# Kernel optimization log

Measured on AMD Instinct MI355X. Metric: run time of the kernel, lower is better.

The kernel has to match this reference:

```python
import jax, jax.numpy as jnp
import numpy as np

B, G, H1, H2, P, A = 8192, 20000, 512, 256, 128, 64


def setup_inputs() -> dict:
    key = jax.random.key(0)
    ks = jax.random.split(key, 9)
    s = lambda k, shape, fan: jax.random.normal(k, shape, jnp.float32) / np.sqrt(fan)
    return {
        "x": jax.random.normal(ks[0], (B, G), jnp.float32),
        "W1": s(ks[1], (H1, G), G),
        "b1": s(ks[2], (H1,), G),
        "W2": s(ks[3], (H2, H1), H1),
        "b2": s(ks[4], (H2,), H1),
        "W3": s(ks[5], (P, H2, A), H2),
        "b3": s(ks[6], (P, A), H2),
        "W4": s(ks[7], (P, A), A),
        "b4": s(ks[8], (P,), A),
    }


def reference(x, W1, b1, W2, b2, W3, b3, W4, b4):
    # shared trunk: two dense layers with ReLU (torch Linear: y = x @ W.T + b)
    h = jax.nn.relu(x @ W1.T + b1)          # [B, 512]
    h = jax.nn.relu(h @ W2.T + b2)          # [B, 256]
    # per-protein heads, batched over the protein dim P (replaces python loop)
    a = jax.nn.relu(jnp.einsum("bh,pha->bpa", h, W3) + b3)  # [B, P, A]
    out = jnp.einsum("bpa,pa->bp", a, W4) + b4               # [B, P]
    return out
```

## Files before the change

kernel.cpp:

```cpp
#include <hip/hip_runtime.h>
#include <hip/hip_bf16.h>
#include <stdint.h>

typedef unsigned short u16;
typedef __attribute__((ext_vector_type(8))) short short8;
typedef __attribute__((ext_vector_type(8))) u16   u16x8;
typedef __attribute__((ext_vector_type(4))) u16   u16x4;
typedef __attribute__((ext_vector_type(4))) float f32x4;

#define B_DIM  8192
#define G_DIM  20000
#define H1_DIM 512
#define H2_DIM 256
#define P_DIM  128
#define A_DIM  64
#define SPLITK 8
#define NKT_ALL 625

union Frag { short8 s; u16x8 u; };

__device__ __forceinline__ u16 f2b(float f) {
  union { __hip_bfloat16 b; u16 u; } c;
  c.b = __float2bfloat16(f);
  return c.u;
}

__device__ __forceinline__ void gld16(const void* g, void* l) {
  __builtin_amdgcn_global_load_lds(
      (const __attribute__((address_space(1))) void*)g,
      (__attribute__((address_space(3))) void*)l, 16, 0, 0);
}

__global__ void k_convert(const float* __restrict__ src, u16* __restrict__ dst, int n4) {
  int i = blockIdx.x * 256 + threadIdx.x;
  if (i >= n4) return;
  f32x4 v = ((const f32x4*)src)[i];
  u16x4 o;
  o[0] = f2b(v[0]); o[1] = f2b(v[1]);
  o[2] = f2b(v[2]); o[3] = f2b(v[3]);
  ((u16x4*)dst)[i] = o;
}

__global__ void k_convert_w1frag(const float* __restrict__ W1, u16* __restrict__ W1f) {
  int ot = blockIdx.x * 256 + threadIdx.x;
  if (ot >= (H1_DIM / 16) * NKT_ALL * 64) return;
  int rowblk = ot / (NKT_ALL * 64);
  int rem    = ot - rowblk * (NKT_ALL * 64);
  int kt     = rem >> 6;
  int lane   = rem & 63;
  int row = rowblk * 16 + (lane & 15);
  int col = kt * 32 + (lane >> 4) * 8;
  const float* src = W1 + (size_t)row * G_DIM + col;
  f32x4 v0 = *(const f32x4*)src;
  f32x4 v1 = *(const f32x4*)(src + 4);
  u16x8 o;
#pragma unroll
  for (int i = 0; i < 4; ++i) { o[i] = f2b(v0[i]); o[i + 4] = f2b(v1[i]); }
  ((u16x8*)W1f)[ot] = o;
}

__global__ void k_transpose_w3(const float* __restrict__ W3, u16* __restrict__ W3T) {
  int idx = blockIdx.x * 256 + threadIdx.x;
  if (idx >= P_DIM * H2_DIM * A_DIM) return;
  int h = idx & (H2_DIM - 1);
  int a = (idx >> 8) & (A_DIM - 1);
  int p = idx >> 14;
  W3T[idx] = f2b(W3[((size_t)p * H2_DIM + h) * A_DIM + a]);
}

__global__ __launch_bounds__(512, 4)
void k_gemm1(const float* __restrict__ X, const u16* __restrict__ W1f,
             float* __restrict__ partial) {
  const int ks = blockIdx.x & 7;
  const int m0 = (blockIdx.x >> 3) * 64;
  const int kt_begin = (ks == 0) ? 0 : (ks * 78 + 1);
  const int nkt = (ks == 0) ? 79 : 78;

  const int tid  = threadIdx.x;
  const int lane = tid & 63;
  const int w    = tid >> 6;
  const int c15 = lane & 15, j4 = lane >> 4;
  const int w4 = w * 4;

  __shared__ u16 lsA[2][64 * 32];

  const int aRow = tid >> 3;
  const int aG   = tid & 7;
  const int aPhysU16 = aRow * 32 + (((aG >> 1) ^ ((aRow >> 1) & 3)) << 3) + ((aG & 1) << 2);
  const float* aSrc0 = X + (size_t)(m0 + aRow) * G_DIM + aG * 4;

  f32x4 zero = {0.f, 0.f, 0.f, 0.f};
  f32x4 acc[4][4];
#pragma unroll
  for (int m = 0; m < 4; ++m)
#pragma unroll
    for (int n = 0; n < 4; ++n) acc[m][n] = zero;

  auto ktc = [&](int t) { return kt_begin + (t < nkt ? t : nkt - 1); };

  auto loadA = [&](int kt, f32x4& ar) {
    ar = *(const f32x4*)(aSrc0 + (size_t)kt * 32);
  };
  auto writeA = [&](int buf, const f32x4& ar) {
    u16x4 o;
    o[0] = f2b(ar[0]); o[1] = f2b(ar[1]); o[2] = f2b(ar[2]); o[3] = f2b(ar[3]);
    *(u16x4*)&lsA[buf][aPhysU16] = o;
  };

  f32x4 arE, arO;

  loadA(ktc(0), arE);
  loadA(ktc(1), arO);
  writeA(0, arE);
  asm volatile("s_waitcnt vmcnt(1) lgkmcnt(0)" ::: "memory");
  __builtin_amdgcn_s_barrier();
  __builtin_amdgcn_sched_barrier(0);

  auto body = [&](int t, int buf, f32x4& arLoad, const f32x4& arWrite) {
    const int kt = kt_begin + t;
    Frag bfr[4];
#pragma unroll
    for (int n = 0; n < 4; ++n)
      bfr[n].s = *(const short8*)(W1f + ((size_t)((w4 + n) * NKT_ALL + kt) * 64 + lane) * 8);
    loadA(ktc(t + 2), arLoad);

    Frag afr[4];
#pragma unroll
    for (int m = 0; m < 4; ++m) {
      int row = m * 16 + c15;
      int phys = j4 ^ ((row >> 1) & 3);
      afr[m].s = *(const short8*)&lsA[buf][row * 32 + phys * 8];
    }
    writeA(buf ^ 1, arWrite);

#pragma unroll
    for (int m = 0; m < 4; ++m)
#pragma unroll
      for (int n = 0; n < 4; ++n)
        acc[m][n] = __builtin_amdgcn_mfma_f32_16x16x32_bf16(afr[m].s, bfr[n].s, acc[m][n], 0, 0, 0);

    asm volatile("s_waitcnt vmcnt(1) lgkmcnt(0)" ::: "memory");
    __builtin_amdgcn_s_barrier();
    __builtin_amdgcn_sched_barrier(0);
  };

  int t = 0;
  for (; t + 1 < nkt; t += 2) {
    body(t,     0, arE, arO);
    body(t + 1, 1, arO, arE);
  }
  if (t < nkt) body(t, 0, arE, arO);

  float* outp = partial + ((size_t)ks * B_DIM + m0) * H1_DIM;
#pragma unroll
  for (int m = 0; m < 4; ++m)
#pragma unroll
    for (int n = 0; n < 4; ++n)
#pragma unroll
      for (int r = 0; r < 4; ++r) {
        int row = m * 16 + j4 * 4 + r;
        int col = w * 64 + n * 16 + c15;
        outp[(size_t)row * H1_DIM + col] = acc[m][n][r];
      }
}

__global__ void k_reduce1(const float* __restrict__ partial, const float* __restrict__ b1,
                          u16* __restrict__ h1b) {
  const int n4 = B_DIM * H1_DIM / 4;
  int i = blockIdx.x * 256 + threadIdx.x;
  if (i >= n4) return;
  f32x4 s = ((const f32x4*)partial)[i];
#pragma unroll
  for (int k = 1; k < SPLITK; ++k) {
    f32x4 v = ((const f32x4*)partial)[(size_t)k * n4 + i];
    s[0] += v[0]; s[1] += v[1]; s[2] += v[2]; s[3] += v[3];
  }
  f32x4 bb = ((const f32x4*)b1)[i & (H1_DIM / 4 - 1)];
  u16x4 o;
#pragma unroll
  for (int j = 0; j < 4; ++j)
    o[j] = f2b(fmaxf(s[j] + bb[j], 0.f));
  ((u16x4*)h1b)[i] = o;
}

__global__ __launch_bounds__(256, 2)
void k_gemm2(const u16* __restrict__ h1b, const u16* __restrict__ W2b,
             const float* __restrict__ b2, u16* __restrict__ h2b) {
  const int m0 = blockIdx.x * 128;
  const int n0 = blockIdx.y * 64;
  const int tid  = threadIdx.x;
  const int lane = tid & 63;
  const int wid  = tid >> 6;
  const int wr = wid >> 1, wc = wid & 1;
  const int c15 = lane & 15, j4 = lane >> 4;

  __shared__ u16 lsA[2][128 * 32];
  __shared__ u16 lsB[2][64 * 32];

  f32x4 zero = {0.f, 0.f, 0.f, 0.f};
  f32x4 acc[4][2];
#pragma unroll
  for (int m = 0; m < 4; ++m) { acc[m][0] = zero; acc[m][1] = zero; }

  auto stage = [&](int buf, int kt) {
    const int k0 = kt * 32;
#pragma unroll
    for (int c = 0; c < 2; ++c) {
      int lin = c * 256 + tid;
      int row = lin >> 2, slot = lin & 3;
      int gslot = slot ^ ((row >> 1) & 3);
      gld16(h1b + (size_t)(m0 + row) * H1_DIM + k0 + gslot * 8, &lsA[buf][lin * 8]);
    }
    {
      int lin = tid;
      int row = lin >> 2, slot = lin & 3;
      int gslot = slot ^ ((row >> 1) & 3);
      gld16(W2b + (size_t)(n0 + row) * H1_DIM + k0 + gslot * 8, &lsB[buf][lin * 8]);
    }
  };

  stage(0, 0);
  __syncthreads();
  int buf = 0;
  const int nkt = H1_DIM / 32;
  for (int t = 0; t < nkt; ++t) {
    if (t + 1 < nkt) stage(buf ^ 1, t + 1);
    Frag bfr[2];
#pragma unroll
    for (int n = 0; n < 2; ++n) {
      int row = wc * 32 + n * 16 + c15;
      int slot = j4 ^ ((row >> 1) & 3);
      bfr[n].s = *(const short8*)&lsB[buf][row * 32 + slot * 8];
    }
    Frag afr[4];
#pragma unroll
    for (int m = 0; m < 4; ++m) {
      int row = wr * 64 + m * 16 + c15;
      int slot = j4 ^ ((row >> 1) & 3);
      afr[m].s = *(const short8*)&lsA[buf][row * 32 + slot * 8];
    }
#pragma unroll
    for (int m = 0; m < 4; ++m)
#pragma unroll
      for (int n = 0; n < 2; ++n)
        acc[m][n] = __builtin_amdgcn_mfma_f32_16x16x32_bf16(afr[m].s, bfr[n].s, acc[m][n], 0, 0, 0);
    __syncthreads();
    buf ^= 1;
  }

  float b2v[2];
  b2v[0] = b2[n0 + wc * 32 + c15];
  b2v[1] = b2[n0 + wc * 32 + 16 + c15];
#pragma unroll
  for (int m = 0; m < 4; ++m)
#pragma unroll
    for (int n = 0; n < 2; ++n)
#pragma unroll
      for (int r = 0; r < 4; ++r) {
        int row = m0 + wr * 64 + m * 16 + j4 * 4 + r;
        int col = n0 + wc * 32 + n * 16 + c15;
        h2b[(size_t)row * H2_DIM + col] = f2b(fmaxf(acc[m][n][r] + b2v[n], 0.f));
      }
}

__global__ __launch_bounds__(256, 2)
void k_heads(const u16* __restrict__ h2b, const u16* __restrict__ W3T,
             const float* __restrict__ b3, const float* __restrict__ W4,
             const float* __restrict__ b4, float* __restrict__ out) {
  const int m0 = blockIdx.x * 128;
  const int p0 = blockIdx.y * 2;
  const int tid  = threadIdx.x;
  const int lane = tid & 63;
  const int wid  = tid >> 6;
  const int wr = wid >> 1, wc = wid & 1;
  const int c15 = lane & 15, j4 = lane >> 4;

  __shared__ u16 lsA[2][128 * 64];
  __shared__ u16 lsB[2][128 * 64];

  f32x4 zero = {0.f, 0.f, 0.f, 0.f};
  f32x4 acc[4][4];
#pragma unroll
  for (int m = 0; m < 4; ++m)
#pragma unroll
    for (int n = 0; n < 4; ++n) acc[m][n] = zero;

  auto stage = [&](int buf, int kt) {
    const int k0 = kt * 64;
#pragma unroll
    for (int c = 0; c < 4; ++c) {
      int lin = c * 256 + tid;
      int row = lin >> 3, slot = lin & 7;
      int gslot = slot ^ (row & 7);
      gld16(h2b + (size_t)(m0 + row) * H2_DIM + k0 + gslot * 8, &lsA[buf][lin * 8]);
    }
#pragma unroll
    for (int c = 0; c < 4; ++c) {
      int lin = c * 256 + tid;
      int row = lin >> 3, slot = lin & 7;
      int gslot = slot ^ (row & 7);
      gld16(W3T + ((size_t)(p0 * 64 + row)) * H2_DIM + k0 + gslot * 8, &lsB[buf][lin * 8]);
    }
  };

  stage(0, 0);
  __syncthreads();
  int buf = 0;
  const int nkt = H2_DIM / 64;
  for (int t = 0; t < nkt; ++t) {
    if (t + 1 < nkt) stage(buf ^ 1, t + 1);
#pragma unroll
    for (int kk = 0; kk < 2; ++kk) {
      Frag bfr[4];
#pragma unroll
      for (int n = 0; n < 4; ++n) {
        int row = wc * 64 + n * 16 + c15;
        int slot = (kk * 4 + j4) ^ (row & 7);
        bfr[n].s = *(const short8*)&lsB[buf][row * 64 + slot * 8];
      }
      Frag afr[4];
#pragma unroll
      for (int m = 0; m < 4; ++m) {
        int row = wr * 64 + m * 16 + c15;
        int slot = (kk * 4 + j4) ^ (row & 7);
        afr[m].s = *(const short8*)&lsA[buf][row * 64 + slot * 8];
      }
#pragma unroll
      for (int m = 0; m < 4; ++m)
#pragma unroll
        for (int n = 0; n < 4; ++n)
          acc[m][n] = __builtin_amdgcn_mfma_f32_16x16x32_bf16(afr[m].s, bfr[n].s, acc[m][n], 0, 0, 0);
    }
    __syncthreads();
    buf ^= 1;
  }

  const int p = p0 + wc;
  float w4v[4], b3v[4];
#pragma unroll
  for (int n = 0; n < 4; ++n) {
    w4v[n] = W4[p * A_DIM + n * 16 + c15];
    b3v[n] = b3[p * A_DIM + n * 16 + c15];
  }
  const float b4v = b4[p];

  float s[4][4];
#pragma unroll
  for (int m = 0; m < 4; ++m)
#pragma unroll
    for (int r = 0; r < 4; ++r) s[m][r] = 0.f;
#pragma unroll
  for (int m = 0; m < 4; ++m)
#pragma unroll
    for (int n = 0; n < 4; ++n)
#pragma unroll
      for (int r = 0; r < 4; ++r) {
        float v = fmaxf(acc[m][n][r] + b3v[n], 0.f);
        s[m][r] += v * w4v[n];
      }
#pragma unroll
  for (int m = 0; m < 4; ++m)
#pragma unroll
    for (int r = 0; r < 4; ++r) {
      float v = s[m][r];
      v += __shfl_xor(v, 1);
      v += __shfl_xor(v, 2);
      v += __shfl_xor(v, 4);
      v += __shfl_xor(v, 8);
      s[m][r] = v;
    }
  if (c15 == 0) {
#pragma unroll
    for (int m = 0; m < 4; ++m)
#pragma unroll
      for (int r = 0; r < 4; ++r) {
        int row = m0 + wr * 64 + m * 16 + j4 * 4 + r;
        out[(size_t)row * P_DIM + p] = s[m][r] + b4v;
      }
  }
}

extern "C" void kernel_launch(void* const* d_in, const int* in_sizes, int n_in,
                              void* d_out, int out_size, void* d_ws, size_t ws_size,
                              hipStream_t stream) {
  const float* x  = (const float*)d_in[0];
  const float* W1 = (const float*)d_in[1];
  const float* b1 = (const float*)d_in[2];
  const float* W2 = (const float*)d_in[3];
  const float* b2 = (const float*)d_in[4];
  const float* W3 = (const float*)d_in[5];
  const float* b3 = (const float*)d_in[6];
  const float* W4 = (const float*)d_in[7];
  const float* b4 = (const float*)d_in[8];
  float* out = (float*)d_out;

  char* ws = (char*)d_ws;
  u16*   W1f  = (u16*)(ws);
  u16*   W2b  = (u16*)(ws + 20480000);
  u16*   W3T  = (u16*)(ws + 20742144);
  u16*   h1b  = (u16*)(ws + 24936448);
  u16*   h2b  = (u16*)(ws + 33325056);
  float* part = (float*)(ws + 37519360);

  k_convert_w1frag<<<dim3((1280000 + 255) / 256), dim3(256), 0, stream>>>(W1, W1f);
  k_convert<<<dim3(131072 / 4 / 256), dim3(256), 0, stream>>>(W2, W2b, 131072 / 4);
  k_transpose_w3<<<dim3(2097152 / 256), dim3(256), 0, stream>>>(W3, W3T);

  k_gemm1<<<dim3(128 * SPLITK), dim3(512), 0, stream>>>(x, W1f, part);
  k_reduce1<<<dim3(B_DIM * H1_DIM / 4 / 256), dim3(256), 0, stream>>>(part, b1, h1b);
  k_gemm2<<<dim3(64, 4), dim3(256), 0, stream>>>(h1b, W2b, b2, h2b);
  k_heads<<<dim3(64, 64), dim3(256), 0, stream>>>(h2b, W3T, b3, W4, b4, out);
}
```

Before: 374.3 us.

## Double the GEMM1 K-step per barrier and software-pipeline W1 fragment loads

Restructures the split-K GEMM1 main loop so each iteration stages a 64-wide K slab of X in LDS (two 32-wide k-tiles) using a new 8-way XOR swizzle. This halves the number of block barriers. It also double-buffers the B (W1) fragments in registers, so the next tile's weights load while the current MFMAs run. It uses more LDS and VGPRs, and the fixed 39-iteration count with a tail case for nkt==79 must match the split exactly.

```diff
diff --git a/kernel.cpp b/kernel.cpp
--- a/kernel.cpp
+++ b/kernel.cpp
@@ -82,12 +82,12 @@
   const int c15 = lane & 15, j4 = lane >> 4;
   const int w4 = w * 4;
 
-  __shared__ u16 lsA[2][64 * 32];
+  __shared__ u16 lsA[2][64 * 64];
 
   const int aRow = tid >> 3;
   const int aG   = tid & 7;
-  const int aPhysU16 = aRow * 32 + (((aG >> 1) ^ ((aRow >> 1) & 3)) << 3) + ((aG & 1) << 2);
-  const float* aSrc0 = X + (size_t)(m0 + aRow) * G_DIM + aG * 4;
+  const int aPhysU16 = aRow * 64 + ((aG ^ (aRow & 7)) * 8);
+  const float* aSrc0 = X + (size_t)(m0 + aRow) * G_DIM + aG * 8;
 
   f32x4 zero = {0.f, 0.f, 0.f, 0.f};
   f32x4 acc[4][4];
@@ -96,60 +96,84 @@
 #pragma unroll
     for (int n = 0; n < 4; ++n) acc[m][n] = zero;
 
-  auto ktc = [&](int t) { return kt_begin + (t < nkt ? t : nkt - 1); };
-
-  auto loadA = [&](int kt, f32x4& ar) {
-    ar = *(const f32x4*)(aSrc0 + (size_t)kt * 32);
-  };
-  auto writeA = [&](int buf, const f32x4& ar) {
-    u16x4 o;
-    o[0] = f2b(ar[0]); o[1] = f2b(ar[1]); o[2] = f2b(ar[2]); o[3] = f2b(ar[3]);
-    *(u16x4*)&lsA[buf][aPhysU16] = o;
-  };
-
-  f32x4 arE, arO;
-
-  loadA(ktc(0), arE);
-  loadA(ktc(1), arO);
-  writeA(0, arE);
-  asm volatile("s_waitcnt vmcnt(1) lgkmcnt(0)" ::: "memory");
+  auto loadB = [&](int kt, Frag* br) {
+#pragma unroll
+    for (int n = 0; n < 4; ++n)
+      br[n].s = *(const short8*)(W1f + ((size_t)((w4 + n) * NKT_ALL + kt) * 64 + lane) * 8);
+  };
+  f32x4 ar0, ar1;
+  auto loadA = [&](int kt) {
+    const float* src = aSrc0 + (size_t)kt * 32;
+    ar0 = *(const f32x4*)src;
+    ar1 = *(const f32x4*)(src + 4);
+  };
+  auto writeA = [&](int buf) {
+    u16x8 o;
+#pragma unroll
+    for (int i = 0; i < 4; ++i) { o[i] = f2b(ar0[i]); o[i + 4] = f2b(ar1[i]); }
+    *(u16x8*)&lsA[buf][aPhysU16] = o;
+  };
+  auto readAfr = [&](int buf, int half, Frag* afr) {
+#pragma unroll
+    for (int m = 0; m < 4; ++m) {
+      int row = m * 16 + c15;
+      int g = half * 4 + j4;
+      int phys = g ^ (row & 7);
+      afr[m].s = *(const short8*)&lsA[buf][row * 64 + phys * 8];
+    }
+  };
+
+  Frag bfrE[4], bfrO[4];
+
+  loadA(kt_begin);
+  loadB(kt_begin, bfrE);
+  writeA(0);
+  asm volatile("s_waitcnt lgkmcnt(0)" ::: "memory");
   __builtin_amdgcn_s_barrier();
   __builtin_amdgcn_sched_barrier(0);
 
-  auto body = [&](int t, int buf, f32x4& arLoad, const f32x4& arWrite) {
-    const int kt = kt_begin + t;
-    Frag bfr[4];
-#pragma unroll
-    for (int n = 0; n < 4; ++n)
-      bfr[n].s = *(const short8*)(W1f + ((size_t)((w4 + n) * NKT_ALL + kt) * 64 + lane) * 8);
-    loadA(ktc(t + 2), arLoad);
+  const int nsuper = 39;
+  for (int T = 0; T < nsuper; ++T) {
+    const int buf = T & 1;
+    const int kt0 = kt_begin + 2 * T;
+    const int ktN = 2 * (T + 1);
+    const int ktNext = kt_begin + ((ktN < nkt) ? ktN : (nkt - 1));
+
+    loadA(ktNext);
+    loadB(kt0 + 1, bfrO);
 
     Frag afr[4];
-#pragma unroll
-    for (int m = 0; m < 4; ++m) {
-      int row = m * 16 + c15;
-      int phys = j4 ^ ((row >> 1) & 3);
-      afr[m].s = *(const short8*)&lsA[buf][row * 32 + phys * 8];
-    }
-    writeA(buf ^ 1, arWrite);
-
+    readAfr(buf, 0, afr);
 #pragma unroll
     for (int m = 0; m < 4; ++m)
 #pragma unroll
       for (int n = 0; n < 4; ++n)
-        acc[m][n] = __builtin_amdgcn_mfma_f32_16x16x32_bf16(afr[m].s, bfr[n].s, acc[m][n], 0, 0, 0);
-
-    asm volatile("s_waitcnt vmcnt(1) lgkmcnt(0)" ::: "memory");
+        acc[m][n] = __builtin_amdgcn_mfma_f32_16x16x32_bf16(afr[m].s, bfrE[n].s, acc[m][n], 0, 0, 0);
+
+    loadB(ktNext, bfrE);
+
+    readAfr(buf, 1, afr);
+#pragma unroll
+    for (int m = 0; m < 4; ++m)
+#pragma unroll
+      for (int n = 0; n < 4; ++n)
+        acc[m][n] = __builtin_amdgcn_mfma_f32_16x16x32_bf16(afr[m].s, bfrO[n].s, acc[m][n], 0, 0, 0);
+
+    writeA(buf ^ 1);
+    asm volatile("s_waitcnt lgkmcnt(0)" ::: "memory");
     __builtin_amdgcn_s_barrier();
     __builtin_amdgcn_sched_barrier(0);
-  };
-
-  int t = 0;
-  for (; t + 1 < nkt; t += 2) {
-    body(t,     0, arE, arO);
-    body(t + 1, 1, arO, arE);
-  }
-  if (t < nkt) body(t, 0, arE, arO);
+  }
+
+  if (nkt == 79) {
+    Frag afr[4];
+    readAfr(1, 0, afr);
+#pragma unroll
+    for (int m = 0; m < 4; ++m)
+#pragma unroll
+      for (int n = 0; n < 4; ++n)
+        acc[m][n] = __builtin_amdgcn_mfma_f32_16x16x32_bf16(afr[m].s, bfrE[n].s, acc[m][n], 0, 0, 0);
+  }
 
   float* outp = partial + ((size_t)ks * B_DIM + m0) * H1_DIM;
 #pragma unroll
```

After: 373.2 us. About the same (-0.3%).
